# Kernel tuning notes

Hardware: AMD Instinct MI355X
Metric: run time of the kernel (lower is better)

Reference implementation:

```python
import jax, jax.numpy as jnp
import numpy as np

HIDDEN = 2048
NUM_HEADS = 32
NUM_KV_HEADS = 8
HEAD_DIM = HIDDEN // NUM_HEADS          # 64
Q_PER_KV = NUM_HEADS // NUM_KV_HEADS    # 4
KV_SIZE = HIDDEN * NUM_KV_HEADS // NUM_HEADS  # 512
BATCH, SEQ = 2, 2048


def setup_inputs() -> dict:
    key = jax.random.key(0)
    ks = jax.random.split(key, 10)
    s = 0.02
    return {
        "x": jax.random.normal(ks[0], (BATCH, SEQ, HIDDEN), jnp.float32),
        "attention_mask": jnp.zeros((BATCH, SEQ), jnp.float32),
        "Wq": jax.random.normal(ks[1], (HIDDEN, HIDDEN), jnp.float32) * s,
        "bq": jnp.zeros((HIDDEN,), jnp.float32),
        "Wk": jax.random.normal(ks[2], (HIDDEN, KV_SIZE), jnp.float32) * s,
        "bk": jnp.zeros((KV_SIZE,), jnp.float32),
        "Wv": jax.random.normal(ks[3], (HIDDEN, KV_SIZE), jnp.float32) * s,
        "bv": jnp.zeros((KV_SIZE,), jnp.float32),
        "Wo": jax.random.normal(ks[4], (HIDDEN, HIDDEN), jnp.float32) * s,
        "bo": jnp.zeros((HIDDEN,), jnp.float32),
    }


def reference(x, attention_mask, Wq, bq, Wk, bk, Wv, bv, Wo, bo):
    b, s, _ = x.shape
    q = x @ Wq + bq                                  # [b,s,H]
    k = x @ Wk + bk                                  # [b,s,kv_size]
    v = x @ Wv + bv
    # q -> [b, kv_heads, q_per_kv, s, head_dim]
    q = q.reshape(b, s, NUM_KV_HEADS, Q_PER_KV, HEAD_DIM).transpose(0, 2, 3, 1, 4)
    # k, v -> [b, kv_heads, s, head_dim]
    k = k.reshape(b, s, NUM_KV_HEADS, HEAD_DIM).transpose(0, 2, 1, 3)
    v = v.reshape(b, s, NUM_KV_HEADS, HEAD_DIM).transpose(0, 2, 1, 3)
    scale = 1.0 / jnp.sqrt(jnp.float32(HEAD_DIM))
    scores = jnp.einsum('bhqsd,bhkd->bhqsk', q, k) * scale   # [b,h,qpk,s,s]
    scores = scores + attention_mask.reshape(b, 1, 1, 1, s)
    attn = jax.nn.softmax(scores, axis=-1)
    out = jnp.einsum('bhqsk,bhkd->bhqsd', attn, v)           # [b,h,qpk,s,d]
    out = out.transpose(0, 3, 1, 2, 4).reshape(b, s, HIDDEN)
    return out @ Wo + bo
```

## Files before the change

kernel.cpp:

```cpp
#include <hip/hip_runtime.h>

typedef __attribute__((ext_vector_type(8))) short short8;
typedef __attribute__((ext_vector_type(4))) float floatx4;

#define B_ 2
#define S_ 2048
#define H_ 2048
#define LOG2E 1.44269504088896f

#define MFMA(a, b, c) __builtin_amdgcn_mfma_f32_16x16x32_bf16(a, b, c, 0, 0, 0)

__device__ __forceinline__ unsigned short f2bf(float f) {
    unsigned int x = __builtin_bit_cast(unsigned int, f);
    unsigned int r = x + 0x7FFFu + ((x >> 16) & 1u);
    return (unsigned short)(r >> 16);
}

__device__ __forceinline__ void gload_lds16(const unsigned short* g, unsigned short* l) {
    __builtin_amdgcn_global_load_lds(
        (const __attribute__((address_space(1))) void*)g,
        (__attribute__((address_space(3))) void*)l, 16, 0, 0);
}

__global__ __launch_bounds__(256) void conv_f2b(const float* __restrict__ in,
                                                unsigned short* __restrict__ out, int n4) {
    int i = blockIdx.x * 256 + threadIdx.x;
    if (i < n4) {
        float4 v = ((const float4*)in)[i];
        ushort4 o;
        o.x = f2bf(v.x); o.y = f2bf(v.y); o.z = f2bf(v.z); o.w = f2bf(v.w);
        ((ushort4*)out)[i] = o;
    }
}

__global__ __launch_bounds__(256) void tr_f2b(const float* __restrict__ in,
                                              unsigned short* __restrict__ out,
                                              int R, int C) {
    __shared__ unsigned short t[32][33];
    int c0 = blockIdx.x * 32, r0 = blockIdx.y * 32;
    int tx = threadIdx.x & 31, ty = threadIdx.x >> 5;
#pragma unroll
    for (int i = 0; i < 32; i += 8)
        t[ty + i][tx] = f2bf(in[(size_t)(r0 + ty + i) * C + c0 + tx]);
    __syncthreads();
#pragma unroll
    for (int i = 0; i < 32; i += 8)
        out[(size_t)(c0 + ty + i) * R + r0 + tx] = t[tx][ty + i];
}

__global__ __launch_bounds__(256) void tr_wqkv(const float* __restrict__ Wq,
                                               const float* __restrict__ Wk,
                                               const float* __restrict__ Wv,
                                               unsigned short* __restrict__ WqkvT) {
    __shared__ unsigned short t[32][33];
    int bx = blockIdx.x;
    const float* src; int C, c0, orow;
    if (bx < 64)      { src = Wq; C = 2048; c0 = bx * 32;        orow = bx * 32; }
    else if (bx < 80) { src = Wk; C = 512;  c0 = (bx - 64) * 32; orow = 2048 + (bx - 64) * 32; }
    else              { src = Wv; C = 512;  c0 = (bx - 80) * 32; orow = 2560 + (bx - 80) * 32; }
    int r0 = blockIdx.y * 32;
    int tx = threadIdx.x & 31, ty = threadIdx.x >> 5;
#pragma unroll
    for (int i = 0; i < 32; i += 8)
        t[ty + i][tx] = f2bf(src[(size_t)(r0 + ty + i) * C + c0 + tx]);
    __syncthreads();
#pragma unroll
    for (int i = 0; i < 32; i += 8)
        WqkvT[(size_t)(orow + ty + i) * 2048 + r0 + tx] = t[tx][ty + i];
}

__global__ __launch_bounds__(256) void tr_bf16(const unsigned short* __restrict__ in,
                                               unsigned short* __restrict__ out,
                                               int R, int C, int ipitch,
                                               size_t ibs, size_t obs) {
    __shared__ unsigned short t[32][33];
    in += (size_t)blockIdx.z * ibs; out += (size_t)blockIdx.z * obs;
    int c0 = blockIdx.x * 32, r0 = blockIdx.y * 32;
    int tx = threadIdx.x & 31, ty = threadIdx.x >> 5;
#pragma unroll
    for (int i = 0; i < 32; i += 8)
        t[ty + i][tx] = in[(size_t)(r0 + ty + i) * ipitch + c0 + tx];
    __syncthreads();
#pragma unroll
    for (int i = 0; i < 32; i += 8)
        out[(size_t)(c0 + ty + i) * R + r0 + tx] = t[tx][ty + i];
}

template <bool OUT_F32>
__global__ __launch_bounds__(256) void gemm_bt(const unsigned short* __restrict__ A,
                                               const unsigned short* __restrict__ Bt,
                                               const float* __restrict__ b0,
                                               const float* __restrict__ b1,
                                               const float* __restrict__ b2,
                                               int s1, int s2,
                                               void* __restrict__ Cv,
                                               int M, int N, int K) {
    __shared__ unsigned short As[128 * 64];
    __shared__ unsigned short Bs[128 * 64];
    const int t = threadIdx.x;
    const int lane = t & 63;
    const int wave = t >> 6;
    const int qlane = lane & 15;
    const int quad = lane >> 4;
    const int wm = (wave >> 1) * 64;
    const int wn = (wave & 1) * 64;
    const int bm = blockIdx.y * 128;
    const int bn = blockIdx.x * 128;
    const int srow = t >> 3;
    const int scc = (t & 7) * 8;
    const int gc8 = (((t & 7) ^ (2 * ((t >> 5) & 3))) * 8);
    const int rsw = 2 * (qlane >> 2);

    floatx4 acc[4][4] = {};

    for (int k0 = 0; k0 < K; k0 += 64) {
        __syncthreads();
#pragma unroll
        for (int r = 0; r < 4; ++r) {
            int row = r * 32 + srow;
            gload_lds16(A + (size_t)(bm + row) * K + k0 + gc8, &As[row * 64 + scc]);
        }
#pragma unroll
        for (int r = 0; r < 4; ++r) {
            int row = r * 32 + srow;
            gload_lds16(Bt + (size_t)(bn + row) * K + k0 + gc8, &Bs[row * 64 + scc]);
        }
        __syncthreads();
#pragma unroll
        for (int kk = 0; kk < 2; ++kk) {
            short8 a[4], b[4];
#pragma unroll
            for (int i = 0; i < 4; ++i)
                a[i] = *(const short8*)&As[(wm + i * 16 + qlane) * 64 + ((kk * 4 + quad) ^ rsw) * 8];
#pragma unroll
            for (int j = 0; j < 4; ++j)
                b[j] = *(const short8*)&Bs[(wn + j * 16 + qlane) * 64 + ((kk * 4 + quad) ^ rsw) * 8];
#pragma unroll
            for (int i = 0; i < 4; ++i)
#pragma unroll
                for (int j = 0; j < 4; ++j)
                    acc[i][j] = MFMA(a[i], b[j], acc[i][j]);
        }
    }
#pragma unroll
    for (int j = 0; j < 4; ++j) {
        int col = bn + wn + j * 16 + qlane;
        int cc = col; const float* bp = b0;
        if (col >= s2)      { bp = b2; cc = col - s2; }
        else if (col >= s1) { bp = b1; cc = col - s1; }
        float bvv = bp[cc];
#pragma unroll
        for (int i = 0; i < 4; ++i) {
            int row0 = bm + wm + i * 16 + quad * 4;
#pragma unroll
            for (int r = 0; r < 4; ++r) {
                float v = acc[i][j][r] + bvv;
                if (OUT_F32)
                    ((float*)Cv)[(size_t)(row0 + r) * N + col] = v;
                else
                    ((unsigned short*)Cv)[(size_t)(row0 + r) * N + col] = f2bf(v);
            }
        }
    }
}

__global__ __launch_bounds__(256, 3) void attn_kernel(const unsigned short* __restrict__ qkv,
                                                      const unsigned short* __restrict__ vtb,
                                                      const float* __restrict__ mask,
                                                      unsigned short* __restrict__ ob) {
    const int qt = blockIdx.x;
    const int head = blockIdx.y;
    const int b = blockIdx.z;
    const int kvh = head >> 2;
    const int qcol = head * 64;
    const int kcol = 2048 + kvh * 64;
    const int vch = kvh * 64;
    const int q0 = qt * 128;
    const int t = threadIdx.x;
    const int lane = t & 63;
    const int wave = t >> 6;
    const int qlane = lane & 15;
    const int quad = lane >> 4;
    const int wr = wave * 32;

    __shared__ unsigned short Ks[2][64 * 64];
    __shared__ unsigned short Vts[2][64 * 64];
    __shared__ unsigned short Ps[128 * 64];

    const int gc8 = (((t & 7) ^ (2 * ((t >> 5) & 3))) * 8);
    const int rsw = 2 * (qlane >> 2);
    const float scale2 = 0.125f * LOG2E;

    short8 aq[2][2];
#pragma unroll
    for (int mi = 0; mi < 2; ++mi)
#pragma unroll
        for (int kk = 0; kk < 2; ++kk)
            aq[mi][kk] = *(const short8*)(qkv +
                (size_t)(b * S_ + q0 + wr + mi * 16 + qlane) * 3072 + qcol + kk * 32 + quad * 8);

    {
        int row = t >> 3;
#pragma unroll
        for (int i = 0; i < 2; ++i) {
            int rr = row + 32 * i;
            gload_lds16(qkv + (size_t)(b * S_ + rr) * 3072 + kcol + gc8,
                        &Ks[0][(rr * 8 + (t & 7)) * 8]);
            gload_lds16(vtb + (size_t)(b * 512 + vch + rr) * S_ + gc8,
                        &Vts[0][(rr * 8 + (t & 7)) * 8]);
        }
    }

    short8 ones;
    {
        short v = (qlane == 0) ? (short)0x3F80 : (short)0;
        ones = (short8){v, v, v, v, v, v, v, v};
    }

    floatx4 o[2][4] = {};
    floatx4 osum[2] = {};

    __syncthreads();

    for (int kt = 0; kt < 32; ++kt) {
        const int cur = kt & 1;
        if (kt < 31) {
            const int nxt = cur ^ 1;
            int kn = (kt + 1) * 64;
            int row = t >> 3;
#pragma unroll
            for (int i = 0; i < 2; ++i) {
                int rr = row + 32 * i;
                gload_lds16(qkv + (size_t)(b * S_ + kn + rr) * 3072 + kcol + gc8,
                            &Ks[nxt][(rr * 8 + (t & 7)) * 8]);
                gload_lds16(vtb + (size_t)(b * 512 + vch + rr) * S_ + kn + gc8,
                            &Vts[nxt][(rr * 8 + (t & 7)) * 8]);
            }
        }
        float m2[4];
#pragma unroll
        for (int j = 0; j < 4; ++j)
            m2[j] = mask[(size_t)b * S_ + kt * 64 + j * 16 + qlane] * LOG2E;

        floatx4 s[2][4] = {};
#pragma unroll
        for (int j = 0; j < 4; ++j) {
            short8 bk0 = *(const short8*)&Ks[cur][(j * 16 + qlane) * 64 + ((0 + quad) ^ rsw) * 8];
            short8 bk1 = *(const short8*)&Ks[cur][(j * 16 + qlane) * 64 + ((4 + quad) ^ rsw) * 8];
#pragma unroll
            for (int mi = 0; mi < 2; ++mi) {
                s[mi][j] = MFMA(aq[mi][0], bk0, s[mi][j]);
                s[mi][j] = MFMA(aq[mi][1], bk1, s[mi][j]);
            }
        }

#pragma unroll
        for (int mi = 0; mi < 2; ++mi)
#pragma unroll
            for (int j = 0; j < 4; ++j) {
                int ebase = (wr + mi * 16 + quad * 4) * 64 + 16 * (j ^ quad) + qlane;
#pragma unroll
                for (int r = 0; r < 4; ++r) {
                    float p = __builtin_amdgcn_exp2f(s[mi][j][r] * scale2 + m2[j]);
                    unsigned int u = __builtin_bit_cast(unsigned int, p) + 0x8000u;
                    Ps[ebase + r * 64] = (unsigned short)(u >> 16);
                }
            }

#pragma unroll
        for (int kk = 0; kk < 2; ++kk) {
            short8 ap[2];
#pragma unroll
            for (int mi = 0; mi < 2; ++mi)
                ap[mi] = *(const short8*)&Ps[(wr + mi * 16 + qlane) * 64 + ((kk * 4 + quad) ^ rsw) * 8];
#pragma unroll
            for (int j2 = 0; j2 < 4; ++j2) {
                short8 bv = *(const short8*)&Vts[cur][(j2 * 16 + qlane) * 64 + ((kk * 4 + quad) ^ rsw) * 8];
#pragma unroll
                for (int mi = 0; mi < 2; ++mi)
                    o[mi][j2] = MFMA(ap[mi], bv, o[mi][j2]);
            }
#pragma unroll
            for (int mi = 0; mi < 2; ++mi)
                osum[mi] = MFMA(ap[mi], ones, osum[mi]);
        }

        __syncthreads();
    }

#pragma unroll
    for (int mi = 0; mi < 2; ++mi)
#pragma unroll
        for (int r = 0; r < 4; ++r) {
            float sm = __shfl(osum[mi][r], quad * 16, 64);
            float inv = 1.0f / sm;
            int row = q0 + wr + mi * 16 + quad * 4 + r;
#pragma unroll
            for (int j2 = 0; j2 < 4; ++j2)
                ob[(size_t)(b * S_ + row) * H_ + qcol + j2 * 16 + qlane] = f2bf(o[mi][j2][r] * inv);
        }
}

extern "C" void kernel_launch(void* const* d_in, const int* in_sizes, int n_in,
                              void* d_out, int out_size, void* d_ws, size_t ws_size,
                              hipStream_t stream) {
    const float* x    = (const float*)d_in[0];
    const float* mask = (const float*)d_in[1];
    const float* Wq   = (const float*)d_in[2];
    const float* bq   = (const float*)d_in[3];
    const float* Wk   = (const float*)d_in[4];
    const float* bk   = (const float*)d_in[5];
    const float* Wv   = (const float*)d_in[6];
    const float* bv   = (const float*)d_in[7];
    const float* Wo   = (const float*)d_in[8];
    const float* bo   = (const float*)d_in[9];
    float* out = (float*)d_out;

    unsigned short* ws = (unsigned short*)d_ws;
    unsigned short* x_bf   = ws;
    unsigned short* qkv    = x_bf + (size_t)4096 * 2048;
    unsigned short* vt_buf = qkv + (size_t)4096 * 3072;
    unsigned short* WqkvT  = vt_buf + (size_t)2 * 512 * 2048;
    unsigned short* WoT    = WqkvT;
    unsigned short* a_buf  = x_bf;

    const int BIG = 1 << 30;
    dim3 blk(256);
    conv_f2b<<<dim3(4096 * 2048 / 4 / 256), blk, 0, stream>>>(x, x_bf, 4096 * 2048 / 4);
    tr_wqkv<<<dim3(96, 64), blk, 0, stream>>>(Wq, Wk, Wv, WqkvT);
    gemm_bt<false><<<dim3(24, 32), blk, 0, stream>>>(x_bf, WqkvT, bq, bk, bv, 2048, 2560,
                                                     qkv, 4096, 3072, 2048);
    tr_f2b<<<dim3(64, 64), blk, 0, stream>>>(Wo, WoT, 2048, 2048);
    tr_bf16<<<dim3(16, 64, 2), blk, 0, stream>>>(qkv + 2560, vt_buf, 2048, 512, 3072,
                                                 (size_t)2048 * 3072, (size_t)512 * 2048);
    attn_kernel<<<dim3(16, 32, 2), blk, 0, stream>>>(qkv, vt_buf, mask, a_buf);
    gemm_bt<true><<<dim3(16, 32), blk, 0, stream>>>(a_buf, WoT, bo, bo, bo, BIG, BIG,
                                                    out, 4096, 2048, 2048);
}
```

Baseline: 385.5 us.

## Use single-wave attention blocks reading K/V directly from global memory

The attention kernel changes from 256-thread blocks with double-buffered LDS staging of K and V to 64-thread single-wave blocks. Each wave loads K and V^T fragments straight from global memory, relying on the cache, and drops the __syncthreads barriers. Block IDs are remapped so the 4 query heads sharing a KV head, and neighbouring query tiles, run on nearby blocks to improve L2 reuse. The trade-off is loss of the LDS-shared K/V tiles among the four waves, more global/L2 traffic per wave, and less latency hiding from prefetch.

```diff
diff --git a/kernel.cpp b/kernel.cpp
--- a/kernel.cpp
+++ b/kernel.cpp
@@ -164,52 +164,43 @@
     }
 }
 
-__global__ __launch_bounds__(256, 3) void attn_kernel(const unsigned short* __restrict__ qkv,
-                                                      const unsigned short* __restrict__ vtb,
-                                                      const float* __restrict__ mask,
-                                                      unsigned short* __restrict__ ob) {
-    const int qt = blockIdx.x;
-    const int head = blockIdx.y;
-    const int b = blockIdx.z;
-    const int kvh = head >> 2;
+__global__ __launch_bounds__(64, 4) void attn_kernel(const unsigned short* __restrict__ qkv,
+                                                     const unsigned short* __restrict__ vtb,
+                                                     const float* __restrict__ mask,
+                                                     unsigned short* __restrict__ ob) {
+    const int bid = blockIdx.x;
+    const int pair = (bid & 7) | (((bid >> 8) & 1) << 3);
+    const int b = pair >> 3;
+    const int kvh = pair & 7;
+    const int idx = ((bid >> 3) & 31) | (((bid >> 9) & 7) << 5);
+    const int qsub = idx & 3;
+    const int qt = idx >> 2;
+    const int head = kvh * 4 + qsub;
     const int qcol = head * 64;
     const int kcol = 2048 + kvh * 64;
     const int vch = kvh * 64;
-    const int q0 = qt * 128;
-    const int t = threadIdx.x;
-    const int lane = t & 63;
-    const int wave = t >> 6;
+    const int q0 = qt * 32;
+
+    const int lane = threadIdx.x;
     const int qlane = lane & 15;
     const int quad = lane >> 4;
-    const int wr = wave * 32;
-
-    __shared__ unsigned short Ks[2][64 * 64];
-    __shared__ unsigned short Vts[2][64 * 64];
-    __shared__ unsigned short Ps[128 * 64];
-
-    const int gc8 = (((t & 7) ^ (2 * ((t >> 5) & 3))) * 8);
+
+    __shared__ unsigned short Ps[32 * 64];
+
     const int rsw = 2 * (qlane >> 2);
     const float scale2 = 0.125f * LOG2E;
 
+    const unsigned short* kbase = qkv + (size_t)b * S_ * 3072 + kcol;
+    const unsigned short* vbase = vtb + (size_t)(b * 512 + vch) * S_;
+    const float* mbase = mask + (size_t)b * S_;
+
     short8 aq[2][2];
 #pragma unroll
     for (int mi = 0; mi < 2; ++mi)
 #pragma unroll
         for (int kk = 0; kk < 2; ++kk)
             aq[mi][kk] = *(const short8*)(qkv +
-                (size_t)(b * S_ + q0 + wr + mi * 16 + qlane) * 3072 + qcol + kk * 32 + quad * 8);
-
-    {
-        int row = t >> 3;
-#pragma unroll
-        for (int i = 0; i < 2; ++i) {
-            int rr = row + 32 * i;
-            gload_lds16(qkv + (size_t)(b * S_ + rr) * 3072 + kcol + gc8,
-                        &Ks[0][(rr * 8 + (t & 7)) * 8]);
-            gload_lds16(vtb + (size_t)(b * 512 + vch + rr) * S_ + gc8,
-                        &Vts[0][(rr * 8 + (t & 7)) * 8]);
-        }
-    }
+                (size_t)(b * S_ + q0 + mi * 16 + qlane) * 3072 + qcol + kk * 32 + quad * 8);
 
     short8 ones;
     {
@@ -220,33 +211,13 @@
     floatx4 o[2][4] = {};
     floatx4 osum[2] = {};
 
-    __syncthreads();
-
     for (int kt = 0; kt < 32; ++kt) {
-        const int cur = kt & 1;
-        if (kt < 31) {
-            const int nxt = cur ^ 1;
-            int kn = (kt + 1) * 64;
-            int row = t >> 3;
-#pragma unroll
-            for (int i = 0; i < 2; ++i) {
-                int rr = row + 32 * i;
-                gload_lds16(qkv + (size_t)(b * S_ + kn + rr) * 3072 + kcol + gc8,
-                            &Ks[nxt][(rr * 8 + (t & 7)) * 8]);
-                gload_lds16(vtb + (size_t)(b * 512 + vch + rr) * S_ + kn + gc8,
-                            &Vts[nxt][(rr * 8 + (t & 7)) * 8]);
-            }
-        }
-        float m2[4];
-#pragma unroll
-        for (int j = 0; j < 4; ++j)
-            m2[j] = mask[(size_t)b * S_ + kt * 64 + j * 16 + qlane] * LOG2E;
-
         floatx4 s[2][4] = {};
 #pragma unroll
         for (int j = 0; j < 4; ++j) {
-            short8 bk0 = *(const short8*)&Ks[cur][(j * 16 + qlane) * 64 + ((0 + quad) ^ rsw) * 8];
-            short8 bk1 = *(const short8*)&Ks[cur][(j * 16 + qlane) * 64 + ((4 + quad) ^ rsw) * 8];
+            const unsigned short* kr = kbase + (size_t)(kt * 64 + j * 16 + qlane) * 3072 + quad * 8;
+            short8 bk0 = *(const short8*)kr;
+            short8 bk1 = *(const short8*)(kr + 32);
 #pragma unroll
             for (int mi = 0; mi < 2; ++mi) {
                 s[mi][j] = MFMA(aq[mi][0], bk0, s[mi][j]);
@@ -254,11 +225,16 @@
             }
         }
 
+        float m2[4];
+#pragma unroll
+        for (int j = 0; j < 4; ++j)
+            m2[j] = mbase[kt * 64 + j * 16 + qlane] * LOG2E;
+
 #pragma unroll
         for (int mi = 0; mi < 2; ++mi)
 #pragma unroll
             for (int j = 0; j < 4; ++j) {
-                int ebase = (wr + mi * 16 + quad * 4) * 64 + 16 * (j ^ quad) + qlane;
+                int ebase = (mi * 16 + quad * 4) * 64 + 16 * (j ^ quad) + qlane;
 #pragma unroll
                 for (int r = 0; r < 4; ++r) {
                     float p = __builtin_amdgcn_exp2f(s[mi][j][r] * scale2 + m2[j]);
@@ -272,10 +248,11 @@
             short8 ap[2];
 #pragma unroll
             for (int mi = 0; mi < 2; ++mi)
-                ap[mi] = *(const short8*)&Ps[(wr + mi * 16 + qlane) * 64 + ((kk * 4 + quad) ^ rsw) * 8];
+                ap[mi] = *(const short8*)&Ps[(mi * 16 + qlane) * 64 + ((kk * 4 + quad) ^ rsw) * 8];
 #pragma unroll
             for (int j2 = 0; j2 < 4; ++j2) {
-                short8 bv = *(const short8*)&Vts[cur][(j2 * 16 + qlane) * 64 + ((kk * 4 + quad) ^ rsw) * 8];
+                short8 bv = *(const short8*)(vbase + (size_t)(j2 * 16 + qlane) * S_ +
+                                             kt * 64 + kk * 32 + quad * 8);
 #pragma unroll
                 for (int mi = 0; mi < 2; ++mi)
                     o[mi][j2] = MFMA(ap[mi], bv, o[mi][j2]);
@@ -284,8 +261,6 @@
             for (int mi = 0; mi < 2; ++mi)
                 osum[mi] = MFMA(ap[mi], ones, osum[mi]);
         }
-
-        __syncthreads();
     }
 
 #pragma unroll
@@ -294,7 +269,7 @@
         for (int r = 0; r < 4; ++r) {
             float sm = __shfl(osum[mi][r], quad * 16, 64);
             float inv = 1.0f / sm;
-            int row = q0 + wr + mi * 16 + quad * 4 + r;
+            int row = q0 + mi * 16 + quad * 4 + r;
 #pragma unroll
             for (int j2 = 0; j2 < 4; ++j2)
                 ob[(size_t)(b * S_ + row) * H_ + qcol + j2 * 16 + qlane] = f2bf(o[mi][j2][r] * inv);
@@ -333,7 +308,7 @@
     tr_f2b<<<dim3(64, 64), blk, 0, stream>>>(Wo, WoT, 2048, 2048);
     tr_bf16<<<dim3(16, 64, 2), blk, 0, stream>>>(qkv + 2560, vt_buf, 2048, 512, 3072,
                                                  (size_t)2048 * 3072, (size_t)512 * 2048);
-    attn_kernel<<<dim3(16, 32, 2), blk, 0, stream>>>(qkv, vt_buf, mask, a_buf);
+    attn_kernel<<<dim3(4096), dim3(64), 0, stream>>>(qkv, vt_buf, mask, a_buf);
     gemm_bt<true><<<dim3(16, 32), blk, 0, stream>>>(a_buf, WoT, bo, bo, bo, BIG, BIG,
                                                     out, 4096, 2048, 2048);
 }
```

Measured after the change: 500.1 us. 1.3x slower.

## Fuse prep/transpose kernels and halve attention P buffer for higher occupancy

Applied to the files above, without the earlier changes.

Merges the x conversion and the QKV weight transpose into one launch, and the Wo transpose and V transpose into another, cutting launch count from seven to five. In the attention kernel the P tile staging buffer shrinks from 128x64 to 64x64. Each wave now processes its two 16-row sub-tiles one after another, reusing the same 16 LDS rows, and launch bounds ask for 4 blocks per SM instead of 3. This lowers LDS use and raises occupancy, at the cost of more serialized LDS writes and reads per wave and a tighter register budget.

```diff
diff --git a/kernel.cpp b/kernel.cpp
--- a/kernel.cpp
+++ b/kernel.cpp
@@ -22,68 +22,70 @@
         (__attribute__((address_space(3))) void*)l, 16, 0, 0);
 }
 
-__global__ __launch_bounds__(256) void conv_f2b(const float* __restrict__ in,
-                                                unsigned short* __restrict__ out, int n4) {
-    int i = blockIdx.x * 256 + threadIdx.x;
-    if (i < n4) {
-        float4 v = ((const float4*)in)[i];
+__global__ __launch_bounds__(256) void prep(const float* __restrict__ x,
+                                            unsigned short* __restrict__ x_bf,
+                                            const float* __restrict__ Wq,
+                                            const float* __restrict__ Wk,
+                                            const float* __restrict__ Wv,
+                                            unsigned short* __restrict__ WqkvT) {
+    __shared__ unsigned short tl[32][33];
+    int bid = blockIdx.x;
+    if (bid < 8192) {
+        int i = bid * 256 + threadIdx.x;
+        float4 v = ((const float4*)x)[i];
         ushort4 o;
         o.x = f2bf(v.x); o.y = f2bf(v.y); o.z = f2bf(v.z); o.w = f2bf(v.w);
-        ((ushort4*)out)[i] = o;
-    }
-}
-
-__global__ __launch_bounds__(256) void tr_f2b(const float* __restrict__ in,
-                                              unsigned short* __restrict__ out,
-                                              int R, int C) {
-    __shared__ unsigned short t[32][33];
-    int c0 = blockIdx.x * 32, r0 = blockIdx.y * 32;
-    int tx = threadIdx.x & 31, ty = threadIdx.x >> 5;
-#pragma unroll
-    for (int i = 0; i < 32; i += 8)
-        t[ty + i][tx] = f2bf(in[(size_t)(r0 + ty + i) * C + c0 + tx]);
-    __syncthreads();
-#pragma unroll
-    for (int i = 0; i < 32; i += 8)
-        out[(size_t)(c0 + ty + i) * R + r0 + tx] = t[tx][ty + i];
-}
-
-__global__ __launch_bounds__(256) void tr_wqkv(const float* __restrict__ Wq,
-                                               const float* __restrict__ Wk,
-                                               const float* __restrict__ Wv,
-                                               unsigned short* __restrict__ WqkvT) {
-    __shared__ unsigned short t[32][33];
-    int bx = blockIdx.x;
+        ((ushort4*)x_bf)[i] = o;
+        return;
+    }
+    int id = bid - 8192;
+    int bx = id % 96, by = id / 96;
     const float* src; int C, c0, orow;
     if (bx < 64)      { src = Wq; C = 2048; c0 = bx * 32;        orow = bx * 32; }
     else if (bx < 80) { src = Wk; C = 512;  c0 = (bx - 64) * 32; orow = 2048 + (bx - 64) * 32; }
     else              { src = Wv; C = 512;  c0 = (bx - 80) * 32; orow = 2560 + (bx - 80) * 32; }
-    int r0 = blockIdx.y * 32;
+    int r0 = by * 32;
     int tx = threadIdx.x & 31, ty = threadIdx.x >> 5;
 #pragma unroll
     for (int i = 0; i < 32; i += 8)
-        t[ty + i][tx] = f2bf(src[(size_t)(r0 + ty + i) * C + c0 + tx]);
+        tl[ty + i][tx] = f2bf(src[(size_t)(r0 + ty + i) * C + c0 + tx]);
     __syncthreads();
 #pragma unroll
     for (int i = 0; i < 32; i += 8)
-        WqkvT[(size_t)(orow + ty + i) * 2048 + r0 + tx] = t[tx][ty + i];
-}
-
-__global__ __launch_bounds__(256) void tr_bf16(const unsigned short* __restrict__ in,
-                                               unsigned short* __restrict__ out,
-                                               int R, int C, int ipitch,
-                                               size_t ibs, size_t obs) {
-    __shared__ unsigned short t[32][33];
-    in += (size_t)blockIdx.z * ibs; out += (size_t)blockIdx.z * obs;
-    int c0 = blockIdx.x * 32, r0 = blockIdx.y * 32;
+        WqkvT[(size_t)(orow + ty + i) * 2048 + r0 + tx] = tl[tx][ty + i];
+}
+
+__global__ __launch_bounds__(256) void tr2(const float* __restrict__ Wo,
+                                           unsigned short* __restrict__ WoT,
+                                           const unsigned short* __restrict__ qkv,
+                                           unsigned short* __restrict__ vt) {
+    __shared__ unsigned short tl[32][33];
+    int bid = blockIdx.x;
     int tx = threadIdx.x & 31, ty = threadIdx.x >> 5;
+    if (bid < 4096) {
+        int bx = bid & 63, by = bid >> 6;
+        int c0 = bx * 32, r0 = by * 32;
+#pragma unroll
+        for (int i = 0; i < 32; i += 8)
+            tl[ty + i][tx] = f2bf(Wo[(size_t)(r0 + ty + i) * 2048 + c0 + tx]);
+        __syncthreads();
+#pragma unroll
+        for (int i = 0; i < 32; i += 8)
+            WoT[(size_t)(c0 + ty + i) * 2048 + r0 + tx] = tl[tx][ty + i];
+        return;
+    }
+    int id = bid - 4096;
+    int bx = id & 15, by = (id >> 4) & 63, bz = id >> 10;
+    const unsigned short* in = qkv + 2560 + (size_t)bz * 2048 * 3072;
+    unsigned short* out = vt + (size_t)bz * 512 * 2048;
+    int c0 = bx * 32, r0 = by * 32;
 #pragma unroll
     for (int i = 0; i < 32; i += 8)
-        t[ty + i][tx] = in[(size_t)(r0 + ty + i) * ipitch + c0 + tx];
+        tl[ty + i][tx] = in[(size_t)(r0 + ty + i) * 3072 + c0 + tx];
     __syncthreads();
 #pragma unroll
     for (int i = 0; i < 32; i += 8)
-        out[(size_t)(c0 + ty + i) * R + r0 + tx] = t[tx][ty + i];
+        out[(size_t)(c0 + ty + i) * 2048 + r0 + tx] = tl[tx][ty + i];
 }
 
 template <bool OUT_F32>
@@ -164,7 +166,7 @@
     }
 }
 
-__global__ __launch_bounds__(256, 3) void attn_kernel(const unsigned short* __restrict__ qkv,
+__global__ __launch_bounds__(256, 4) void attn_kernel(const unsigned short* __restrict__ qkv,
                                                       const unsigned short* __restrict__ vtb,
                                                       const float* __restrict__ mask,
                                                       unsigned short* __restrict__ ob) {
@@ -185,11 +187,14 @@
 
     __shared__ unsigned short Ks[2][64 * 64];
     __shared__ unsigned short Vts[2][64 * 64];
-    __shared__ unsigned short Ps[128 * 64];
+    __shared__ unsigned short Ps[64 * 64];
 
     const int gc8 = (((t & 7) ^ (2 * ((t >> 5) & 3))) * 8);
     const int rsw = 2 * (qlane >> 2);
     const float scale2 = 0.125f * LOG2E;
+
+    const unsigned short* vbase = vtb + (size_t)(b * 512 + vch) * S_;
+    const float* mbase = mask + (size_t)b * S_;
 
     short8 aq[2][2];
 #pragma unroll
@@ -206,7 +211,7 @@
             int rr = row + 32 * i;
             gload_lds16(qkv + (size_t)(b * S_ + rr) * 3072 + kcol + gc8,
                         &Ks[0][(rr * 8 + (t & 7)) * 8]);
-            gload_lds16(vtb + (size_t)(b * 512 + vch + rr) * S_ + gc8,
+            gload_lds16(vbase + (size_t)rr * S_ + gc8,
                         &Vts[0][(rr * 8 + (t & 7)) * 8]);
         }
     }
@@ -224,6 +229,7 @@
 
     for (int kt = 0; kt < 32; ++kt) {
         const int cur = kt & 1;
+
         if (kt < 31) {
             const int nxt = cur ^ 1;
             int kn = (kt + 1) * 64;
@@ -233,14 +239,14 @@
                 int rr = row + 32 * i;
                 gload_lds16(qkv + (size_t)(b * S_ + kn + rr) * 3072 + kcol + gc8,
                             &Ks[nxt][(rr * 8 + (t & 7)) * 8]);
-                gload_lds16(vtb + (size_t)(b * 512 + vch + rr) * S_ + kn + gc8,
+                gload_lds16(vbase + (size_t)rr * S_ + kn + gc8,
                             &Vts[nxt][(rr * 8 + (t & 7)) * 8]);
             }
         }
         float m2[4];
 #pragma unroll
         for (int j = 0; j < 4; ++j)
-            m2[j] = mask[(size_t)b * S_ + kt * 64 + j * 16 + qlane] * LOG2E;
+            m2[j] = mbase[kt * 64 + j * 16 + qlane] * LOG2E;
 
         floatx4 s[2][4] = {};
 #pragma unroll
@@ -255,10 +261,10 @@
         }
 
 #pragma unroll
-        for (int mi = 0; mi < 2; ++mi)
+        for (int mi = 0; mi < 2; ++mi) {
 #pragma unroll
             for (int j = 0; j < 4; ++j) {
-                int ebase = (wr + mi * 16 + quad * 4) * 64 + 16 * (j ^ quad) + qlane;
+                int ebase = (wave * 16 + quad * 4) * 64 + 16 * (j ^ quad) + qlane;
 #pragma unroll
                 for (int r = 0; r < 4; ++r) {
                     float p = __builtin_amdgcn_exp2f(s[mi][j][r] * scale2 + m2[j]);
@@ -266,23 +272,16 @@
                     Ps[ebase + r * 64] = (unsigned short)(u >> 16);
                 }
             }
-
-#pragma unroll
-        for (int kk = 0; kk < 2; ++kk) {
-            short8 ap[2];
-#pragma unroll
-            for (int mi = 0; mi < 2; ++mi)
-                ap[mi] = *(const short8*)&Ps[(wr + mi * 16 + qlane) * 64 + ((kk * 4 + quad) ^ rsw) * 8];
-#pragma unroll
-            for (int j2 = 0; j2 < 4; ++j2) {
-                short8 bv = *(const short8*)&Vts[cur][(j2 * 16 + qlane) * 64 + ((kk * 4 + quad) ^ rsw) * 8];
-#pragma unroll
-                for (int mi = 0; mi < 2; ++mi)
-                    o[mi][j2] = MFMA(ap[mi], bv, o[mi][j2]);
-            }
-#pragma unroll
-            for (int mi = 0; mi < 2; ++mi)
-                osum[mi] = MFMA(ap[mi], ones, osum[mi]);
+#pragma unroll
+            for (int kk = 0; kk < 2; ++kk) {
+                short8 ap = *(const short8*)&Ps[(wave * 16 + qlane) * 64 + ((kk * 4 + quad) ^ rsw) * 8];
+#pragma unroll
+                for (int j2 = 0; j2 < 4; ++j2) {
+                    short8 bv = *(const short8*)&Vts[cur][(j2 * 16 + qlane) * 64 + ((kk * 4 + quad) ^ rsw) * 8];
+                    o[mi][j2] = MFMA(ap, bv, o[mi][j2]);
+                }
+                osum[mi] = MFMA(ap, ones, osum[mi]);
+            }
         }
 
         __syncthreads();
@@ -326,13 +325,10 @@
 
     const int BIG = 1 << 30;
     dim3 blk(256);
-    conv_f2b<<<dim3(4096 * 2048 / 4 / 256), blk, 0, stream>>>(x, x_bf, 4096 * 2048 / 4);
-    tr_wqkv<<<dim3(96, 64), blk, 0, stream>>>(Wq, Wk, Wv, WqkvT);
+    prep<<<dim3(8192 + 96 * 64), blk, 0, stream>>>(x, x_bf, Wq, Wk, Wv, WqkvT);
     gemm_bt<false><<<dim3(24, 32), blk, 0, stream>>>(x_bf, WqkvT, bq, bk, bv, 2048, 2560,
                                                      qkv, 4096, 3072, 2048);
-    tr_f2b<<<dim3(64, 64), blk, 0, stream>>>(Wo, WoT, 2048, 2048);
-    tr_bf16<<<dim3(16, 64, 2), blk, 0, stream>>>(qkv + 2560, vt_buf, 2048, 512, 3072,
-                                                 (size_t)2048 * 3072, (size_t)512 * 2048);
+    tr2<<<dim3(4096 + 2048), blk, 0, stream>>>(Wo, WoT, qkv, vt_buf);
     attn_kernel<<<dim3(16, 32, 2), blk, 0, stream>>>(qkv, vt_buf, mask, a_buf);
     gemm_bt<true><<<dim3(16, 32), blk, 0, stream>>>(a_buf, WoT, bo, bo, bo, BIG, BIG,
                                                     out, 4096, 2048, 2048);
```

Measured after the change: 368.5 us. -4.4%, faster.
